# Kernel tuning notes

Measured on AMD Instinct MI355X. Metric: run time of the kernel, lower is better.

The kernel has to match this reference:

```python
import jax, jax.numpy as jnp
import numpy as np

D = 512
LD = 2
NTR = 16384
NT = 8192
NCLS = 16

def setup_inputs() -> dict:
    key = jax.random.key(0)
    k1, k2, k3, k4 = jax.random.split(key, 4)
    xtr = jax.random.normal(k1, (NTR, D), dtype=jnp.float32)
    ytr = jax.random.normal(k2, (NTR, NCLS), dtype=jnp.float32)
    xt = jax.random.normal(k3, (NT, D), dtype=jnp.float32)
    # original: A ~ U[0,1)/sqrt(d), shape (ld, d), used as x @ A with A stored (d, ld) here
    A = jax.random.uniform(k4, (D, LD), dtype=jnp.float32) / jnp.sqrt(jnp.float32(D))
    return {"xtr": xtr, "ytr": ytr, "xt": xt, "A": A}

def reference(xtr, ytr, xt, A):
    # low-rank projections: [Nt, ld], [Ntr, ld]
    q = xt @ A
    k = xtr @ A
    # similarity logits [Nt, Ntr], softmax over train points, weighted label agg
    E = jax.nn.softmax(q @ k.T, axis=1)
    return E @ ytr
```

## Files before the change

### kernel.cpp

```cpp
#include <hip/hip_runtime.h>
#include <hip/hip_bf16.h>
#include <math.h>

#define DIM   512
#define NTR   16384
#define NT    8192
#define NCLS  16
#define NROWS (NTR + NT)

#define JS     16
#define JC     (NTR / JS)
#define STEPS  (JC / 32)
#define NSTEPS (NTR / 32)

#define WS_KQ_F    (NROWS * 2)
#define WS_NUMER_F (NT * NCLS)
#define WS_DENOM_F (NT)
#define WS_ZERO_V4 ((WS_NUMER_F + WS_DENOM_F) / 4)

typedef __attribute__((ext_vector_type(8))) short short8;
typedef __attribute__((ext_vector_type(4))) float f32x4;
typedef __attribute__((ext_vector_type(4))) unsigned int uint4v;

static __device__ __forceinline__ short f2bf(float f) {
    unsigned u = __float_as_uint(f);
    return (short)((u + 0x7FFFu + ((u >> 16) & 1u)) >> 16);
}
static __device__ __forceinline__ float bf2f(short h) {
    return __uint_as_float(((unsigned)(unsigned short)h) << 16);
}
static __device__ __forceinline__ unsigned pkbf(float a, float b) {
    unsigned ua = __float_as_uint(a) + 0x8000u;
    unsigned ub = __float_as_uint(b) + 0x8000u;
    return __builtin_amdgcn_perm(ub, ua, 0x07060302);
}

__global__ __launch_bounds__(256) void proj_kernel(
    const float* __restrict__ xtr, const float* __restrict__ xt,
    const float* __restrict__ A, float* __restrict__ kq)
{
    const int wave = threadIdx.x >> 6;
    const int lane = threadIdx.x & 63;
    const int row0 = blockIdx.x * 8 + wave * 2;

    const float* x0 = (row0 < NTR) ? (xtr + (size_t)row0 * DIM)
                                   : (xt + (size_t)(row0 - NTR) * DIM);
    const float* x1 = (row0 + 1 < NTR) ? (xtr + (size_t)(row0 + 1) * DIM)
                                       : (xt + (size_t)(row0 + 1 - NTR) * DIM);
    float a00 = 0.f, a01 = 0.f, a10 = 0.f, a11 = 0.f;
#pragma unroll
    for (int t = 0; t < 2; ++t) {
        const int d = lane * 4 + t * 256;
        float4 u = *(const float4*)(x0 + d);
        float4 v = *(const float4*)(x1 + d);
        float4 A0 = *(const float4*)(A + 2 * d);
        float4 A1 = *(const float4*)(A + 2 * d + 4);
        a00 += u.x * A0.x + u.y * A0.z + u.z * A1.x + u.w * A1.z;
        a01 += u.x * A0.y + u.y * A0.w + u.z * A1.y + u.w * A1.w;
        a10 += v.x * A0.x + v.y * A0.z + v.z * A1.x + v.w * A1.z;
        a11 += v.x * A0.y + v.y * A0.w + v.z * A1.y + v.w * A1.w;
    }
#pragma unroll
    for (int off = 32; off >= 1; off >>= 1) {
        a00 += __shfl_xor(a00, off, 64);
        a01 += __shfl_xor(a01, off, 64);
        a10 += __shfl_xor(a10, off, 64);
        a11 += __shfl_xor(a11, off, 64);
    }
    if (lane == 0)
        *(float4*)(kq + row0 * 2) = make_float4(a00, a01, a10, a11);
}

__global__ __launch_bounds__(256) void prepy_kernel(
    const float* __restrict__ ytr, short* __restrict__ yfh,
    short* __restrict__ yfl, float* __restrict__ zbase)
{
    const int idx  = blockIdx.x * 256 + threadIdx.x;
    float4 z = make_float4(0.f, 0.f, 0.f, 0.f);
    for (int p = idx; p < WS_ZERO_V4; p += NSTEPS * 64)
        ((float4*)zbase)[p] = z;

    const int l    = idx & 63;
    const int s    = idx >> 6;
    const int cls  = l & 15;
    const int jb   = s * 32 + (l >> 4) * 8;
    short8 hi, lo;
#pragma unroll
    for (int t = 0; t < 8; ++t) {
        float v = ytr[(size_t)(jb + t) * NCLS + cls];
        short h = f2bf(v);
        hi[t] = h;
        lo[t] = f2bf(v - bf2f(h));
    }
    ((short8*)yfh)[idx] = hi;
    ((short8*)yfl)[idx] = lo;
}

__global__ __launch_bounds__(256) void simmain_kernel(
    const float* __restrict__ kq, const short* __restrict__ yfh,
    const short* __restrict__ yfl, float* __restrict__ numer,
    float* __restrict__ denom)
{
    __shared__ float ks[JC * 2];

    const int tid  = threadIdx.x;
    const int wave = tid >> 6;
    const int lane = tid & 63;
    const int j0   = blockIdx.y * JC;

    {
        const float4* src = (const float4*)(kq + 2 * j0);
        float4* dst = (float4*)ks;
#pragma unroll
        for (int p = 0; p < (JC * 2 / 4) / 256; ++p)
            dst[tid + 256 * p] = src[tid + 256 * p];
    }
    __syncthreads();

    const int i0   = (blockIdx.x * 4 + wave) * 16;
    const int m    = lane & 15;
    const int quad = lane >> 4;

    const float2 qv = *(const float2*)(kq + 2 * (NTR + i0 + m));
    const float q0 = qv.x * 1.4426950408889634f;
    const float q1 = qv.y * 1.4426950408889634f;

    f32x4 acc  = {0.f, 0.f, 0.f, 0.f};
    f32x4 acc2 = {0.f, 0.f, 0.f, 0.f};
    short8 ones;
#pragma unroll
    for (int t = 0; t < 8; ++t) ones[t] = (short)0x3F80;

    const short8* __restrict__ yhp = ((const short8*)yfh) + (size_t)blockIdx.y * (STEPS * 64) + lane;
    const short8* __restrict__ ylp = ((const short8*)yfl) + (size_t)blockIdx.y * (STEPS * 64) + lane;
    const float4* __restrict__ kx  = ((const float4*)ks) + quad * 4;

#pragma unroll 4
    for (int s = 0; s < STEPS; ++s) {
        const short8 yh = yhp[s * 64];
        const short8 yl = ylp[s * 64];
        const float4* kp = kx + s * 16;
        const float4 ka = kp[0], kb = kp[1], kc = kp[2], kd = kp[3];

        const float e0 = exp2f(fmaf(q1, ka.y, q0 * ka.x));
        const float e1 = exp2f(fmaf(q1, ka.w, q0 * ka.z));
        const float e2 = exp2f(fmaf(q1, kb.y, q0 * kb.x));
        const float e3 = exp2f(fmaf(q1, kb.w, q0 * kb.z));
        const float e4 = exp2f(fmaf(q1, kc.y, q0 * kc.x));
        const float e5 = exp2f(fmaf(q1, kc.w, q0 * kc.z));
        const float e6 = exp2f(fmaf(q1, kd.y, q0 * kd.x));
        const float e7 = exp2f(fmaf(q1, kd.w, q0 * kd.z));

        uint4v ep;
        ep[0] = pkbf(e0, e1); ep[1] = pkbf(e2, e3);
        ep[2] = pkbf(e4, e5); ep[3] = pkbf(e6, e7);
        const short8 eb = __builtin_bit_cast(short8, ep);

        acc  = __builtin_amdgcn_mfma_f32_16x16x32_bf16(yh,   eb, acc,  0, 0, 0);
        acc  = __builtin_amdgcn_mfma_f32_16x16x32_bf16(yl,   eb, acc,  0, 0, 0);
        acc2 = __builtin_amdgcn_mfma_f32_16x16x32_bf16(ones, eb, acc2, 0, 0, 0);
    }

    float* nrow = numer + (size_t)(i0 + m) * NCLS + quad * 4;
#pragma unroll
    for (int r = 0; r < 4; ++r)
        atomicAdd(nrow + r, acc[r]);
    if (quad == 0)
        atomicAdd(denom + i0 + m, acc2[0]);
}

__global__ __launch_bounds__(256) void finalize_kernel(
    const float* __restrict__ numer, const float* __restrict__ denom,
    float* __restrict__ out)
{
    const int idx = blockIdx.x * 256 + threadIdx.x;
    out[idx] = numer[idx] / denom[idx >> 4];
}

extern "C" void kernel_launch(void* const* d_in, const int* in_sizes, int n_in,
                              void* d_out, int out_size, void* d_ws, size_t ws_size,
                              hipStream_t stream)
{
    const float* xtr = (const float*)d_in[0];
    const float* ytr = (const float*)d_in[1];
    const float* xt  = (const float*)d_in[2];
    const float* A   = (const float*)d_in[3];
    float* out = (float*)d_out;

    float* kq    = (float*)d_ws;
    float* numer = kq + WS_KQ_F;
    float* denom = numer + WS_NUMER_F;
    short* yfh   = (short*)(denom + WS_DENOM_F);
    short* yfl   = yfh + NSTEPS * 64 * 8;

    prepy_kernel<<<(NSTEPS * 64) / 256, 256, 0, stream>>>(ytr, yfh, yfl, numer);
    proj_kernel<<<NROWS / 8, 256, 0, stream>>>(xtr, xt, A, kq);
    simmain_kernel<<<dim3(NT / 64, JS), 256, 0, stream>>>(kq, yfh, yfl, numer, denom);
    finalize_kernel<<<(NT * NCLS) / 256, 256, 0, stream>>>(numer, denom, out);
}
```

Baseline: 135.8 us.

## Merge prep and projection kernels, fold finalize into main via last-block counter

Combines the label-prep and projection kernels into one launch, with each projection wave now handling four rows instead of two so the A loads are reused. The finalize kernel is removed: the last of the JS blocks to finish each row-group, detected with an atomic counter, divides numer by denom and writes the output. exp2f is replaced by the hardware exp2 builtin. This cuts two kernel launches and their gaps, at the cost of threadfences plus a counter in the workspace that must be re-zeroed on every call.

```diff
diff --git a/kernel.cpp b/kernel.cpp
--- a/kernel.cpp
+++ b/kernel.cpp
@@ -13,10 +13,14 @@
 #define STEPS  (JC / 32)
 #define NSTEPS (NTR / 32)
 
+#define PROJ_BLOCKS (NROWS / 16)
+#define PREP_BLOCKS ((NSTEPS * 64) / 256)
+
 #define WS_KQ_F    (NROWS * 2)
 #define WS_NUMER_F (NT * NCLS)
 #define WS_DENOM_F (NT)
-#define WS_ZERO_V4 ((WS_NUMER_F + WS_DENOM_F) / 4)
+#define WS_CNT_F   128
+#define WS_ZERO_V4 ((WS_NUMER_F + WS_DENOM_F + WS_CNT_F) / 4)
 
 typedef __attribute__((ext_vector_type(8))) short short8;
 typedef __attribute__((ext_vector_type(4))) float f32x4;
@@ -35,73 +39,81 @@
     return __builtin_amdgcn_perm(ub, ua, 0x07060302);
 }
 
-__global__ __launch_bounds__(256) void proj_kernel(
+__global__ __launch_bounds__(256) void prep_kernel(
     const float* __restrict__ xtr, const float* __restrict__ xt,
-    const float* __restrict__ A, float* __restrict__ kq)
-{
-    const int wave = threadIdx.x >> 6;
-    const int lane = threadIdx.x & 63;
-    const int row0 = blockIdx.x * 8 + wave * 2;
-
-    const float* x0 = (row0 < NTR) ? (xtr + (size_t)row0 * DIM)
-                                   : (xt + (size_t)(row0 - NTR) * DIM);
-    const float* x1 = (row0 + 1 < NTR) ? (xtr + (size_t)(row0 + 1) * DIM)
-                                       : (xt + (size_t)(row0 + 1 - NTR) * DIM);
-    float a00 = 0.f, a01 = 0.f, a10 = 0.f, a11 = 0.f;
-#pragma unroll
-    for (int t = 0; t < 2; ++t) {
-        const int d = lane * 4 + t * 256;
-        float4 u = *(const float4*)(x0 + d);
-        float4 v = *(const float4*)(x1 + d);
-        float4 A0 = *(const float4*)(A + 2 * d);
-        float4 A1 = *(const float4*)(A + 2 * d + 4);
-        a00 += u.x * A0.x + u.y * A0.z + u.z * A1.x + u.w * A1.z;
-        a01 += u.x * A0.y + u.y * A0.w + u.z * A1.y + u.w * A1.w;
-        a10 += v.x * A0.x + v.y * A0.z + v.z * A1.x + v.w * A1.z;
-        a11 += v.x * A0.y + v.y * A0.w + v.z * A1.y + v.w * A1.w;
-    }
-#pragma unroll
-    for (int off = 32; off >= 1; off >>= 1) {
-        a00 += __shfl_xor(a00, off, 64);
-        a01 += __shfl_xor(a01, off, 64);
-        a10 += __shfl_xor(a10, off, 64);
-        a11 += __shfl_xor(a11, off, 64);
-    }
-    if (lane == 0)
-        *(float4*)(kq + row0 * 2) = make_float4(a00, a01, a10, a11);
-}
-
-__global__ __launch_bounds__(256) void prepy_kernel(
-    const float* __restrict__ ytr, short* __restrict__ yfh,
+    const float* __restrict__ A, const float* __restrict__ ytr,
+    float* __restrict__ kq, short* __restrict__ yfh,
     short* __restrict__ yfl, float* __restrict__ zbase)
 {
-    const int idx  = blockIdx.x * 256 + threadIdx.x;
-    float4 z = make_float4(0.f, 0.f, 0.f, 0.f);
-    for (int p = idx; p < WS_ZERO_V4; p += NSTEPS * 64)
-        ((float4*)zbase)[p] = z;
-
-    const int l    = idx & 63;
-    const int s    = idx >> 6;
-    const int cls  = l & 15;
-    const int jb   = s * 32 + (l >> 4) * 8;
-    short8 hi, lo;
-#pragma unroll
-    for (int t = 0; t < 8; ++t) {
-        float v = ytr[(size_t)(jb + t) * NCLS + cls];
-        short h = f2bf(v);
-        hi[t] = h;
-        lo[t] = f2bf(v - bf2f(h));
-    }
-    ((short8*)yfh)[idx] = hi;
-    ((short8*)yfl)[idx] = lo;
+    const int b = blockIdx.x;
+    if (b < PROJ_BLOCKS) {
+        const int wave = threadIdx.x >> 6;
+        const int lane = threadIdx.x & 63;
+        const int row0 = b * 16 + wave * 4;
+
+        const float* xp[4];
+#pragma unroll
+        for (int r = 0; r < 4; ++r) {
+            const int row = row0 + r;
+            xp[r] = (row < NTR) ? (xtr + (size_t)row * DIM)
+                                : (xt + (size_t)(row - NTR) * DIM);
+        }
+        float a0[4] = {0.f, 0.f, 0.f, 0.f}, a1[4] = {0.f, 0.f, 0.f, 0.f};
+#pragma unroll
+        for (int t = 0; t < 2; ++t) {
+            const int d = lane * 4 + t * 256;
+            float4 A0 = *(const float4*)(A + 2 * d);
+            float4 A1 = *(const float4*)(A + 2 * d + 4);
+#pragma unroll
+            for (int r = 0; r < 4; ++r) {
+                float4 u = *(const float4*)(xp[r] + d);
+                a0[r] += u.x * A0.x + u.y * A0.z + u.z * A1.x + u.w * A1.z;
+                a1[r] += u.x * A0.y + u.y * A0.w + u.z * A1.y + u.w * A1.w;
+            }
+        }
+#pragma unroll
+        for (int off = 32; off >= 1; off >>= 1) {
+#pragma unroll
+            for (int r = 0; r < 4; ++r) {
+                a0[r] += __shfl_xor(a0[r], off, 64);
+                a1[r] += __shfl_xor(a1[r], off, 64);
+            }
+        }
+        if (lane == 0) {
+            *(float4*)(kq + row0 * 2)     = make_float4(a0[0], a1[0], a0[1], a1[1]);
+            *(float4*)(kq + row0 * 2 + 4) = make_float4(a0[2], a1[2], a0[3], a1[3]);
+        }
+    } else {
+        const int idx = (b - PROJ_BLOCKS) * 256 + threadIdx.x;
+        float4 z = make_float4(0.f, 0.f, 0.f, 0.f);
+        for (int p = idx; p < WS_ZERO_V4; p += PREP_BLOCKS * 256)
+            ((float4*)zbase)[p] = z;
+
+        const int l   = idx & 63;
+        const int s   = idx >> 6;
+        const int cls = l & 15;
+        const int jb  = s * 32 + (l >> 4) * 8;
+        short8 hi, lo;
+#pragma unroll
+        for (int t = 0; t < 8; ++t) {
+            float v = ytr[(size_t)(jb + t) * NCLS + cls];
+            short h = f2bf(v);
+            hi[t] = h;
+            lo[t] = f2bf(v - bf2f(h));
+        }
+        ((short8*)yfh)[idx] = hi;
+        ((short8*)yfl)[idx] = lo;
+    }
 }
 
 __global__ __launch_bounds__(256) void simmain_kernel(
     const float* __restrict__ kq, const short* __restrict__ yfh,
     const short* __restrict__ yfl, float* __restrict__ numer,
-    float* __restrict__ denom)
+    float* __restrict__ denom, int* __restrict__ cnt,
+    float* __restrict__ out)
 {
     __shared__ float ks[JC * 2];
+    __shared__ int last_flag;
 
     const int tid  = threadIdx.x;
     const int wave = tid >> 6;
@@ -142,14 +154,14 @@
         const float4* kp = kx + s * 16;
         const float4 ka = kp[0], kb = kp[1], kc = kp[2], kd = kp[3];
 
-        const float e0 = exp2f(fmaf(q1, ka.y, q0 * ka.x));
-        const float e1 = exp2f(fmaf(q1, ka.w, q0 * ka.z));
-        const float e2 = exp2f(fmaf(q1, kb.y, q0 * kb.x));
-        const float e3 = exp2f(fmaf(q1, kb.w, q0 * kb.z));
-        const float e4 = exp2f(fmaf(q1, kc.y, q0 * kc.x));
-        const float e5 = exp2f(fmaf(q1, kc.w, q0 * kc.z));
-        const float e6 = exp2f(fmaf(q1, kd.y, q0 * kd.x));
-        const float e7 = exp2f(fmaf(q1, kd.w, q0 * kd.z));
+        const float e0 = __builtin_amdgcn_exp2f(fmaf(q1, ka.y, q0 * ka.x));
+        const float e1 = __builtin_amdgcn_exp2f(fmaf(q1, ka.w, q0 * ka.z));
+        const float e2 = __builtin_amdgcn_exp2f(fmaf(q1, kb.y, q0 * kb.x));
+        const float e3 = __builtin_amdgcn_exp2f(fmaf(q1, kb.w, q0 * kb.z));
+        const float e4 = __builtin_amdgcn_exp2f(fmaf(q1, kc.y, q0 * kc.x));
+        const float e5 = __builtin_amdgcn_exp2f(fmaf(q1, kc.w, q0 * kc.z));
+        const float e6 = __builtin_amdgcn_exp2f(fmaf(q1, kd.y, q0 * kd.x));
+        const float e7 = __builtin_amdgcn_exp2f(fmaf(q1, kd.w, q0 * kd.z));
 
         uint4v ep;
         ep[0] = pkbf(e0, e1); ep[1] = pkbf(e2, e3);
@@ -167,14 +179,26 @@
         atomicAdd(nrow + r, acc[r]);
     if (quad == 0)
         atomicAdd(denom + i0 + m, acc2[0]);
-}
-
-__global__ __launch_bounds__(256) void finalize_kernel(
-    const float* __restrict__ numer, const float* __restrict__ denom,
-    float* __restrict__ out)
-{
-    const int idx = blockIdx.x * 256 + threadIdx.x;
-    out[idx] = numer[idx] / denom[idx >> 4];
+
+    __threadfence();
+    if (tid == 0)
+        last_flag = (atomicAdd(cnt + blockIdx.x, 1) == JS - 1);
+    __syncthreads();
+    if (last_flag) {
+        __threadfence();
+        const int li = tid >> 2;
+        const int c4 = (tid & 3) * 4;
+        const int gi = blockIdx.x * 64 + li;
+        const float* nr = numer + (size_t)gi * NCLS + c4;
+        float d = __hip_atomic_load(denom + gi, __ATOMIC_RELAXED, __HIP_MEMORY_SCOPE_AGENT);
+        float rd = 1.0f / d;
+        float4 o;
+        o.x = __hip_atomic_load(nr + 0, __ATOMIC_RELAXED, __HIP_MEMORY_SCOPE_AGENT) * rd;
+        o.y = __hip_atomic_load(nr + 1, __ATOMIC_RELAXED, __HIP_MEMORY_SCOPE_AGENT) * rd;
+        o.z = __hip_atomic_load(nr + 2, __ATOMIC_RELAXED, __HIP_MEMORY_SCOPE_AGENT) * rd;
+        o.w = __hip_atomic_load(nr + 3, __ATOMIC_RELAXED, __HIP_MEMORY_SCOPE_AGENT) * rd;
+        *(float4*)(out + (size_t)gi * NCLS + c4) = o;
+    }
 }
 
 extern "C" void kernel_launch(void* const* d_in, const int* in_sizes, int n_in,
@@ -190,11 +214,12 @@
     float* kq    = (float*)d_ws;
     float* numer = kq + WS_KQ_F;
     float* denom = numer + WS_NUMER_F;
-    short* yfh   = (short*)(denom + WS_DENOM_F);
+    int*   cnt   = (int*)(denom + WS_DENOM_F);
+    short* yfh   = (short*)(cnt + WS_CNT_F);
     short* yfl   = yfh + NSTEPS * 64 * 8;
 
-    prepy_kernel<<<(NSTEPS * 64) / 256, 256, 0, stream>>>(ytr, yfh, yfl, numer);
-    proj_kernel<<<NROWS / 8, 256, 0, stream>>>(xtr, xt, A, kq);
-    simmain_kernel<<<dim3(NT / 64, JS), 256, 0, stream>>>(kq, yfh, yfl, numer, denom);
-    finalize_kernel<<<(NT * NCLS) / 256, 256, 0, stream>>>(numer, denom, out);
-}
+    prep_kernel<<<PROJ_BLOCKS + PREP_BLOCKS, 256, 0, stream>>>(
+        xtr, xt, A, ytr, kq, yfh, yfl, numer);
+    simmain_kernel<<<dim3(NT / 64, JS), 256, 0, stream>>>(
+        kq, yfh, yfl, numer, denom, cnt, out);
+}
```

Measured after the change: 248.6 us. +83.1%, slower.
